# Performance work log

Hardware: AMD Instinct MI355X
Metric: run time of the kernel (lower is better)

Reference implementation:

```python
import jax, jax.numpy as jnp
import numpy as np

# SLAYER SRM-alpha kernel: k[n] = (n/tau) * exp(1 - n/tau), k[0] = 0 (Ts = 1).
# Realized exactly as a 2-state linear recurrence instead of an explicit time conv:
#   s1[n] = r*s1[n-1] + x[n];  s2[n] = r*s2[n-1] + r*s1[n];  out[n] = (e/tau)*s2[n-1]
# which reproduces k[n] = n * r**n * e / tau for an impulse.

def _alpha_psp(x, tau):
    r = jnp.float32(np.exp(-1.0 / tau))
    coef = jnp.float32(np.e / tau)
    xT = jnp.moveaxis(x, -1, 0)  # [T,N,C,H,W]
    zeros = jnp.zeros_like(xT[0])
    def step(carry, xt):
        s1, s2 = carry
        out = coef * s2          # kernel value 0 at lag 0
        s1 = r * s1 + xt
        s2 = r * s2 + r * s1
        return (s1, s2), out
    _, out = jax.lax.scan(step, (zeros, zeros), xT)
    return jnp.moveaxis(out, 0, -1)


def _make_spike_fn(theta, tauRho, scaleRho):
    # Hard threshold forward, SLAYER exponential surrogate backward.
    @jax.custom_vjp
    def f(u):
        return (u >= theta).astype(u.dtype)
    def fwd(u):
        return f(u), u
    def bwd(u, g):
        pdf = (scaleRho / tauRho) * jnp.exp(-jnp.abs(u - theta) / (tauRho * theta))
        return (g * pdf,)
    f.defvjp(fwd, bwd)
    return f


def _spike_dynamics(u, theta, tauRef, scaleRef, tauRho, scaleRho):
    # membrane[t] = u[t] + refractory response of past spikes,
    # refKernel[n] = -scaleRef*theta * (n/tauRef) * exp(1 - n/tauRef)
    r = jnp.float32(np.exp(-1.0 / tauRef))
    coef = jnp.float32(-scaleRef * theta * np.e / tauRef)
    spike_fn = _make_spike_fn(theta, tauRho, scaleRho)
    uT = jnp.moveaxis(u, -1, 0)  # [T,N,C,H,W]
    zeros = jnp.zeros_like(uT[0])
    def step(carry, ut):
        s1, s2 = carry
        m = ut + coef * s2       # spike at t does not refract itself (kernel[0]=0)
        s = spike_fn(m)
        s1 = r * s1 + s
        s2 = r * s2 + r * s1
        return (s1, s2), s
    _, out = jax.lax.scan(step, (zeros, zeros), uT)
    return jnp.moveaxis(out, 0, -1)


def _conv2d_time(x, w, pad):
    # SLAYER conv3d with kernel (k,k,1): a 2D conv applied independently per timestep.
    N, C, H, W, T = x.shape
    xb = jnp.moveaxis(x, -1, 1).reshape(N * T, C, H, W)
    y = jax.lax.conv_general_dilated(
        xb, w, (1, 1), [(pad, pad), (pad, pad)],
        dimension_numbers=('NCHW', 'OIHW', 'NCHW'))
    return jnp.moveaxis(y.reshape(N, T, w.shape[0], H, W), 1, -1)


def setup_inputs() -> dict:
    key = jax.random.key(0)
    k1, k2, k3, k4 = jax.random.split(key, 4)
    N, C, H, W, T = 8, 4, 128, 128, 50
    spikeInput = (jax.random.uniform(k1, (N, C, H, W, T)) < 0.1).astype(jnp.float32)
    # weight scales chosen so membranes cross the per-layer thresholds (SLAYER weightScale)
    w1 = jax.random.normal(k2, (4, 4, 5, 5), jnp.float32) * 2.0
    w2 = jax.random.normal(k3, (4, 4, 3, 3), jnp.float32) * 4.0
    w3 = jax.random.normal(k4, (4, 4, 3, 3), jnp.float32) * 8.0
    return {"spikeInput": spikeInput, "w1": w1, "w2": w2, "w3": w3}


def reference(spikeInput, w1, w2, w3):
    s1 = _spike_dynamics(_conv2d_time(_alpha_psp(spikeInput, 1.0), w1, 2),
                         20.0, 1.0, 1.0, 1.0, 10.0)
    s2 = _spike_dynamics(_conv2d_time(_alpha_psp(s1, 2.0), w2, 1),
                         40.0, 2.0, 1.0, 1.0, 10.0)
    # Layer 3 is computed by the original forward but its result is NOT returned
    # (the torch code returns spikes_layer_2). XLA will DCE it.
    s3 = _spike_dynamics(_conv2d_time(_alpha_psp(s2, 4.0), w3, 1),
                         80.0, 4.0, 1.0, 10.0, 100.0)
    return s2
```

## Files before the change

kernel.cpp:

```cpp
#include <hip/hip_runtime.h>


#define TC 10

__global__ __launch_bounds__(256)
void snn_pack(const float* __restrict__ xin, uint2* __restrict__ xmg)
{
    __shared__ unsigned long long bal[4][50];
    const int tid  = threadIdx.x;
    const int lane = tid & 63;
    const int ws   = tid >> 6;
    const size_t wpx = ((size_t)blockIdx.x * 4 + ws) * 64;
    const float* src = xin + wpx * 50;
#pragma unroll 1
    for (int j = 0; j < 50; ++j) {
        float v = src[j * 64 + lane];
        unsigned long long b = __ballot(v != 0.f);
        if (lane == 0) bal[ws][j] = b;
    }
    __syncthreads();
    const int bitpos = lane * 50;
    const int w = bitpos >> 6, s = bitpos & 63;
    unsigned long long m = bal[ws][w] >> s;
    if (s > 14) m |= bal[ws][w + 1] << (64 - s);
    m &= (1ull << 50) - 1;
    xmg[wpx + lane] = make_uint2((unsigned)m, (unsigned)(m >> 32));
}

#define HS1 20
#define HP1 21
__global__ __launch_bounds__(256)
void snn_l1(const uint2* __restrict__ xmg, const float* __restrict__ w1,
            uint2* __restrict__ s1g)
{
    __shared__ __align__(16) uint2 xs[4][HS1 * HP1];
    __shared__ __align__(16) float wL1[400];

    const int tid = threadIdx.x;
    const int n = blockIdx.z, Y0 = blockIdx.y * 16, X0 = blockIdx.x * 16;

    for (int i = tid; i < 400; i += 256) {
        int oc = i & 3, r = i >> 2;
        int ic = r / 25, r2 = r - ic * 25;
        int dy = r2 / 5, dx = r2 - dy * 5;
        wL1[i] = w1[((oc * 4 + ic) * 5 + dy) * 5 + dx];
    }
#pragma unroll
    for (int s = 0; s < 2; ++s) {
        int hp = tid + s * 256;
        if (hp < HS1 * HS1) {
            int hy = hp / HS1, hx = hp - hy * HS1;
            int gy = Y0 + hy - 2, gx = X0 + hx - 2;
            bool ok = gy >= 0 && gy < 128 && gx >= 0 && gx < 128;
            int gi = (gy << 7) + gx;
            int li = hy * HP1 + hx;
#pragma unroll
            for (int c = 0; c < 4; ++c) {
                uint2 v = make_uint2(0u, 0u);
                if (ok) v = xmg[(((size_t)(n * 4 + c)) << 14) + gi];
                xs[c][li] = v;
            }
        }
    }
    __syncthreads();

    const int cy = tid >> 4, cx = tid & 15;
    const int base = cy * HP1 + cx;

    float s1a[4] = {}, s2a[4] = {}, s1b[4] = {}, s2b[4] = {};
    unsigned long long om[4] = {};
    const float R1  = 0.36787944117144233f;
    const float CO1 = 2.7182818284590452f;
    const float CRF = -54.365636569180902f;

    for (int chk = 0; chk < 5; ++chk) {
        const int t0 = chk * TC;
        float a[TC][4];
#pragma unroll
        for (int u = 0; u < TC; ++u) { a[u][0]=0.f; a[u][1]=0.f; a[u][2]=0.f; a[u][3]=0.f; }
#pragma unroll 1
        for (int ic = 0; ic < 4; ++ic) {
            const uint2*  xp = &xs[ic][base];
            const float4* wp = (const float4*)&wL1[ic * 100];
#pragma unroll 1
            for (int dy = 0; dy < 5; ++dy) {
#pragma unroll
                for (int dx = 0; dx < 5; ++dx) {
                    uint2 mv = xp[dx];
                    unsigned long long mm = ((unsigned long long)mv.y << 32) | mv.x;
                    unsigned win = (unsigned)(mm >> t0);
                    float4 w = wp[dx];
#pragma unroll
                    for (int u = 0; u < TC; ++u) {
                        float f = (float)((win >> u) & 1u);
                        a[u][0] = fmaf(f, w.x, a[u][0]);
                        a[u][1] = fmaf(f, w.y, a[u][1]);
                        a[u][2] = fmaf(f, w.z, a[u][2]);
                        a[u][3] = fmaf(f, w.w, a[u][3]);
                    }
                }
                xp += HP1; wp += 5;
            }
        }
        unsigned cm[4] = {0, 0, 0, 0};
#pragma unroll
        for (int u = 0; u < TC; ++u) {
#pragma unroll
            for (int oc = 0; oc < 4; ++oc) {
                float ao  = CO1 * s2a[oc];
                float ns1 = fmaf(R1, s1a[oc], a[u][oc]);
                s1a[oc] = ns1;
                s2a[oc] = fmaf(R1, s2a[oc], R1 * ns1);
                float mv = fmaf(CRF, s2b[oc], ao);
                unsigned b = (mv >= 20.f) ? 1u : 0u;
                float spf = (float)b;
                float nb1 = fmaf(R1, s1b[oc], spf);
                s1b[oc] = nb1;
                s2b[oc] = fmaf(R1, s2b[oc], R1 * nb1);
                cm[oc] |= b << u;
            }
        }
#pragma unroll
        for (int oc = 0; oc < 4; ++oc)
            om[oc] |= (unsigned long long)cm[oc] << t0;
    }

    const int yx = (Y0 + cy) * 128 + X0 + cx;
#pragma unroll
    for (int oc = 0; oc < 4; ++oc)
        s1g[(((size_t)(n * 4 + oc)) << 14) + yx] =
            make_uint2((unsigned)om[oc], (unsigned)(om[oc] >> 32));
}

#define HS2 18
#define HP2 19
__global__ __launch_bounds__(256)
void snn_l2(const uint2* __restrict__ s1g, const float* __restrict__ w2,
            float* __restrict__ out)
{
    __shared__ __align__(16) uint2 ss[4][HS2 * HP2];
    __shared__ __align__(16) float wL2[144];
    __shared__ unsigned long long oml[256 * 4];

    const int tid = threadIdx.x;
    const int n = blockIdx.z, Y0 = blockIdx.y * 16, X0 = blockIdx.x * 16;

    if (tid < 144) {
        int oc = tid & 3, r = tid >> 2;
        int ic = r / 9, r2 = r - ic * 9;
        int dy = r2 / 3, dx = r2 - dy * 3;
        wL2[tid] = w2[((oc * 4 + ic) * 3 + dy) * 3 + dx];
    }
#pragma unroll
    for (int s = 0; s < 2; ++s) {
        int hp = tid + s * 256;
        if (hp < HS2 * HS2) {
            int hy = hp / HS2, hx = hp - hy * HS2;
            int gy = Y0 + hy - 1, gx = X0 + hx - 1;
            bool ok = gy >= 0 && gy < 128 && gx >= 0 && gx < 128;
            int gi = (gy << 7) + gx;
            int li = hy * HP2 + hx;
#pragma unroll
            for (int c = 0; c < 4; ++c) {
                uint2 v = make_uint2(0u, 0u);
                if (ok) v = s1g[(((size_t)(n * 4 + c)) << 14) + gi];
                ss[c][li] = v;
            }
        }
    }
    __syncthreads();

    const int cy = tid >> 4, cx = tid & 15;
    const int base = cy * HP2 + cx;

    float s1c[4] = {}, s2c[4] = {}, s1d[4] = {}, s2d[4] = {};
    unsigned long long om[4] = {};
    const float R2  = 0.60653065971263342f;
    const float CO2 = 1.3591409142295226f;
    const float CRF = -54.365636569180902f;

    for (int chk = 0; chk < 5; ++chk) {
        const int t0 = chk * TC;
        float a[TC][4];
#pragma unroll
        for (int u = 0; u < TC; ++u) { a[u][0]=0.f; a[u][1]=0.f; a[u][2]=0.f; a[u][3]=0.f; }
#pragma unroll 1
        for (int ic = 0; ic < 4; ++ic) {
            const uint2*  sp = &ss[ic][base];
            const float4* wp = (const float4*)&wL2[ic * 36];
#pragma unroll 1
            for (int dy = 0; dy < 3; ++dy) {
#pragma unroll
                for (int dx = 0; dx < 3; ++dx) {
                    uint2 mv = sp[dx];
                    unsigned long long mm = ((unsigned long long)mv.y << 32) | mv.x;
                    unsigned win = (unsigned)(mm >> t0);
                    float4 w = wp[dx];
#pragma unroll
                    for (int u = 0; u < TC; ++u) {
                        float f = (float)((win >> u) & 1u);
                        a[u][0] = fmaf(f, w.x, a[u][0]);
                        a[u][1] = fmaf(f, w.y, a[u][1]);
                        a[u][2] = fmaf(f, w.z, a[u][2]);
                        a[u][3] = fmaf(f, w.w, a[u][3]);
                    }
                }
                sp += HP2; wp += 3;
            }
        }
        unsigned cm[4] = {0, 0, 0, 0};
#pragma unroll
        for (int u = 0; u < TC; ++u) {
#pragma unroll
            for (int oc = 0; oc < 4; ++oc) {
                float ao  = CO2 * s2c[oc];
                float ns1 = fmaf(R2, s1c[oc], a[u][oc]);
                s1c[oc] = ns1;
                s2c[oc] = fmaf(R2, s2c[oc], R2 * ns1);
                float mv = fmaf(CRF, s2d[oc], ao);
                unsigned b = (mv >= 40.f) ? 1u : 0u;
                float spf = (float)b;
                float nd1 = fmaf(R2, s1d[oc], spf);
                s1d[oc] = nd1;
                s2d[oc] = fmaf(R2, s2d[oc], R2 * nd1);
                cm[oc] |= b << u;
            }
        }
#pragma unroll
        for (int oc = 0; oc < 4; ++oc)
            om[oc] |= (unsigned long long)cm[oc] << t0;
    }

#pragma unroll
    for (int oc = 0; oc < 4; ++oc) oml[tid * 4 + oc] = om[oc];
    __syncthreads();

    for (int i = tid; i < 256 * 4 * 25; i += 256) {
        int pc = i / 25;
        int j  = i - pc * 25;
        int p  = pc >> 2, c = pc & 3;
        unsigned long long m = oml[p * 4 + c];
        int py = p >> 4, px = p & 15;
        int k = 2 * j;
        float2 v;
        v.x = (float)((unsigned)(m >> k) & 1u);
        v.y = (float)((unsigned)(m >> (k + 1)) & 1u);
        float* o = out + ((size_t)(((n * 4 + c) << 14) + (Y0 + py) * 128 + X0 + px)) * 50;
        *(float2*)(o + k) = v;
    }
}

#define TW   16
#define TH   8
#define R1S  (TW + 6)
#define R1R  (TH + 6)
#define R1N  (R1S * R1R)
#define R2S  (TW + 2)
#define R2R  (TH + 2)
#define R2N  (R2S * R2R)

__global__ __launch_bounds__(256)
void snn_fused_fb(const float* __restrict__ xin,
                  const float* __restrict__ w1,
                  const float* __restrict__ w2,
                  float* __restrict__ out)
{
    __shared__ __align__(16) uint2    xm[4][R1N];
    __shared__ unsigned               s1m[4][R2N];
    __shared__ __align__(16) float    wL1[400];
    __shared__ __align__(16) float    wL2[144];

    const int tid = threadIdx.x;
    const int n   = blockIdx.z;
    const int Y0  = blockIdx.y * TH;
    const int X0  = blockIdx.x * TW;

    for (int i = tid; i < 400; i += 256) {
        int oc = i & 3, r = i >> 2;
        int ic = r / 25, r2 = r - ic * 25;
        int dy = r2 / 5, dx = r2 - dy * 5;
        wL1[i] = w1[((oc * 4 + ic) * 5 + dy) * 5 + dx];
    }
    if (tid < 144) {
        int oc = tid & 3, r = tid >> 2;
        int ic = r / 9, r2 = r - ic * 9;
        int dy = r2 / 3, dx = r2 - dy * 3;
        wL2[tid] = w2[((oc * 4 + ic) * 3 + dy) * 3 + dx];
    }
#pragma unroll
    for (int s = 0; s < 2; ++s) {
        int hp = tid + s * 256;
        if (hp < R1N) {
            int hy = hp / R1S, hx = hp - hy * R1S;
            int gy = Y0 + hy - 3, gx = X0 + hx - 3;
            bool inimg = gy >= 0 && gy < 128 && gx >= 0 && gx < 128;
#pragma unroll
            for (int c = 0; c < 4; ++c) {
                unsigned m0 = 0, m1 = 0;
                if (inimg) {
                    const float2* p = (const float2*)
                        (xin + ((size_t)(((n * 4 + c) * 128 + gy) * 128 + gx)) * 50);
#pragma unroll
                    for (int j = 0; j < 25; ++j) {
                        float2 v = p[j];
                        unsigned b0 = (v.x != 0.f) ? 1u : 0u;
                        unsigned b1 = (v.y != 0.f) ? 1u : 0u;
                        int k = 2 * j;
                        if (k < 32) m0 |= (b0 << k) | (b1 << (k + 1));
                        else        m1 |= (b0 << (k - 32)) | (b1 << (k - 31));
                    }
                }
                xm[c][hp] = make_uint2(m0, m1);
            }
        }
    }
    const bool cw = (tid < R2N);
    const int cy = tid / R2S;
    const int cx = tid - cy * R2S;
    const bool cin = cw && (Y0 + cy - 1) >= 0 && (Y0 + cy - 1) < 128
                        && (X0 + cx - 1) >= 0 && (X0 + cx - 1) < 128;
    const int xbase = cy * R1S + cx;
    const bool iw = (tid < TW * TH);
    const int iy = tid >> 4, ix = tid & 15;
    const int ibase = iy * R2S + ix;

    float s1a[4] = {}, s2a[4] = {}, s1b[4] = {}, s2b[4] = {};
    float s1c[4] = {}, s2c[4] = {}, s1d[4] = {}, s2d[4] = {};
    unsigned long long om[4] = {};

    const float R1  = 0.36787944117144233f;
    const float CO1 = 2.7182818284590452f;
    const float R2  = 0.60653065971263342f;
    const float CO2 = 1.3591409142295226f;
    const float CRF = -54.365636569180902f;

    __syncthreads();

    for (int chk = 0; chk < 5; ++chk) {
        const int t0 = chk * TC;
        if (cw) {
            float a[TC][4];
#pragma unroll
            for (int u = 0; u < TC; ++u) { a[u][0]=0.f; a[u][1]=0.f; a[u][2]=0.f; a[u][3]=0.f; }
            if (cin) {
#pragma unroll 1
                for (int ic = 0; ic < 4; ++ic) {
                    const uint2*  xp = &xm[ic][xbase];
                    const float4* wp = (const float4*)&wL1[ic * 100];
#pragma unroll 1
                    for (int dy = 0; dy < 5; ++dy) {
#pragma unroll
                        for (int dx = 0; dx < 5; ++dx) {
                            uint2 m = xp[dx];
                            unsigned long long mm =
                                ((unsigned long long)m.y << 32) | m.x;
                            unsigned win = (unsigned)(mm >> t0);
                            float4 w = wp[dx];
#pragma unroll
                            for (int u = 0; u < TC; ++u) {
                                float f = (float)((win >> u) & 1u);
                                a[u][0] = fmaf(f, w.x, a[u][0]);
                                a[u][1] = fmaf(f, w.y, a[u][1]);
                                a[u][2] = fmaf(f, w.z, a[u][2]);
                                a[u][3] = fmaf(f, w.w, a[u][3]);
                            }
                        }
                        xp += R1S; wp += 5;
                    }
                }
            }
            unsigned cm[4] = {0, 0, 0, 0};
#pragma unroll
            for (int u = 0; u < TC; ++u) {
#pragma unroll
                for (int oc = 0; oc < 4; ++oc) {
                    float ao  = CO1 * s2a[oc];
                    float ns1 = fmaf(R1, s1a[oc], a[u][oc]);
                    s1a[oc] = ns1;
                    s2a[oc] = fmaf(R1, s2a[oc], R1 * ns1);
                    float mv = fmaf(CRF, s2b[oc], ao);
                    unsigned b = (mv >= 20.f) ? 1u : 0u;
                    float spf = (float)b;
                    float nb1 = fmaf(R1, s1b[oc], spf);
                    s1b[oc] = nb1;
                    s2b[oc] = fmaf(R1, s2b[oc], R1 * nb1);
                    cm[oc] |= b << u;
                }
            }
            s1m[0][tid] = cm[0];
            s1m[1][tid] = cm[1];
            s1m[2][tid] = cm[2];
            s1m[3][tid] = cm[3];
        }
        __syncthreads();
        if (iw) {
            float a[TC][4];
#pragma unroll
            for (int u = 0; u < TC; ++u) { a[u][0]=0.f; a[u][1]=0.f; a[u][2]=0.f; a[u][3]=0.f; }
#pragma unroll 1
            for (int ic = 0; ic < 4; ++ic) {
                const unsigned* sp = &s1m[ic][ibase];
                const float4*   wp = (const float4*)&wL2[ic * 36];
#pragma unroll 1
                for (int dy = 0; dy < 3; ++dy) {
#pragma unroll
                    for (int dx = 0; dx < 3; ++dx) {
                        unsigned win = sp[dx];
                        float4 w = wp[dx];
#pragma unroll
                        for (int u = 0; u < TC; ++u) {
                            float f = (float)((win >> u) & 1u);
                            a[u][0] = fmaf(f, w.x, a[u][0]);
                            a[u][1] = fmaf(f, w.y, a[u][1]);
                            a[u][2] = fmaf(f, w.z, a[u][2]);
                            a[u][3] = fmaf(f, w.w, a[u][3]);
                        }
                    }
                    sp += R2S; wp += 3;
                }
            }
            unsigned cm[4] = {0, 0, 0, 0};
#pragma unroll
            for (int u = 0; u < TC; ++u) {
#pragma unroll
                for (int oc = 0; oc < 4; ++oc) {
                    float ao  = CO2 * s2c[oc];
                    float ns1 = fmaf(R2, s1c[oc], a[u][oc]);
                    s1c[oc] = ns1;
                    s2c[oc] = fmaf(R2, s2c[oc], R2 * ns1);
                    float mv = fmaf(CRF, s2d[oc], ao);
                    unsigned b = (mv >= 40.f) ? 1u : 0u;
                    float spf = (float)b;
                    float nd1 = fmaf(R2, s1d[oc], spf);
                    s1d[oc] = nd1;
                    s2d[oc] = fmaf(R2, s2d[oc], R2 * nd1);
                    cm[oc] |= b << u;
                }
            }
#pragma unroll
            for (int oc = 0; oc < 4; ++oc)
                om[oc] |= (unsigned long long)cm[oc] << t0;
        }
        __syncthreads();
    }
    if (iw) {
#pragma unroll
        for (int c = 0; c < 4; ++c) {
            float* p = out + ((size_t)(((n * 4 + c) * 128 + (Y0 + iy)) * 128 + (X0 + ix))) * 50;
            unsigned long long m = om[c];
#pragma unroll
            for (int j = 0; j < 25; ++j) {
                int k = 2 * j;
                float2 v;
                v.x = (float)((unsigned)(m >> k) & 1u);
                v.y = (float)((unsigned)(m >> (k + 1)) & 1u);
                *(float2*)(p + k) = v;
            }
        }
    }
}

extern "C" void kernel_launch(void* const* d_in, const int* in_sizes, int n_in,
                              void* d_out, int out_size, void* d_ws, size_t ws_size,
                              hipStream_t stream) {
    (void)in_sizes; (void)n_in; (void)out_size;
    const float* x  = (const float*)d_in[0];
    const float* w1 = (const float*)d_in[1];
    const float* w2 = (const float*)d_in[2];
    float* o = (float*)d_out;

    if (ws_size >= 2u * 4194304u) {
        uint2* xmg = (uint2*)d_ws;
        uint2* s1g = xmg + 524288;
        hipLaunchKernelGGL(snn_pack, dim3(2048), dim3(256), 0, stream, x, xmg);
        hipLaunchKernelGGL(snn_l1, dim3(8, 8, 8), dim3(256), 0, stream, xmg, w1, s1g);
        hipLaunchKernelGGL(snn_l2, dim3(8, 8, 8), dim3(256), 0, stream, s1g, w2, o);
    } else {
        dim3 grid(128 / TW, 128 / TH, 8);
        hipLaunchKernelGGL(snn_fused_fb, grid, dim3(256), 0, stream, x, w1, w2, o);
    }
}
```

Measured before the change: 326.3 us.

## Split input channels across thread pairs and double grid in conv layers

Each pixel in the layer-1 and layer-2 kernels is now handled by two threads. Each thread convolves two of the four input channels, and the partial sums are exchanged with a lane shuffle. Each thread then runs the recurrence for two output channels. Tiles shrink to 16x8 and the grid doubles, so there are more blocks and more waves to hide latency on the 512-block launch. The cost is extra shuffles and more halo reloading per output pixel.

```diff
diff --git a/kernel.cpp b/kernel.cpp
--- a/kernel.cpp
+++ b/kernel.cpp
@@ -27,17 +27,18 @@
     xmg[wpx + lane] = make_uint2((unsigned)m, (unsigned)(m >> 32));
 }
 
-#define HS1 20
+#define HW1 20
+#define HH1 12
 #define HP1 21
 __global__ __launch_bounds__(256)
 void snn_l1(const uint2* __restrict__ xmg, const float* __restrict__ w1,
             uint2* __restrict__ s1g)
 {
-    __shared__ __align__(16) uint2 xs[4][HS1 * HP1];
+    __shared__ __align__(16) uint2 xs[4][HH1 * HP1];
     __shared__ __align__(16) float wL1[400];
 
     const int tid = threadIdx.x;
-    const int n = blockIdx.z, Y0 = blockIdx.y * 16, X0 = blockIdx.x * 16;
+    const int n = blockIdx.z, Y0 = blockIdx.y * 8, X0 = blockIdx.x * 16;
 
     for (int i = tid; i < 400; i += 256) {
         int oc = i & 3, r = i >> 2;
@@ -45,11 +46,10 @@
         int dy = r2 / 5, dx = r2 - dy * 5;
         wL1[i] = w1[((oc * 4 + ic) * 5 + dy) * 5 + dx];
     }
-#pragma unroll
-    for (int s = 0; s < 2; ++s) {
-        int hp = tid + s * 256;
-        if (hp < HS1 * HS1) {
-            int hy = hp / HS1, hx = hp - hy * HS1;
+    {
+        int hp = tid;
+        if (hp < HW1 * HH1) {
+            int hy = hp / HW1, hx = hp - hy * HW1;
             int gy = Y0 + hy - 2, gx = X0 + hx - 2;
             bool ok = gy >= 0 && gy < 128 && gx >= 0 && gx < 128;
             int gi = (gy << 7) + gx;
@@ -64,11 +64,13 @@
     }
     __syncthreads();
 
-    const int cy = tid >> 4, cx = tid & 15;
-    const int base = cy * HP1 + cx;
-
-    float s1a[4] = {}, s2a[4] = {}, s1b[4] = {}, s2b[4] = {};
-    unsigned long long om[4] = {};
+    const int h  = tid & 1;
+    const int px = tid >> 1;
+    const int py = px >> 4, pxx = px & 15;
+    const int base = py * HP1 + pxx;
+
+    float s1a[2] = {}, s2a[2] = {}, s1b[2] = {}, s2b[2] = {};
+    unsigned long long om[2] = {};
     const float R1  = 0.36787944117144233f;
     const float CO1 = 2.7182818284590452f;
     const float CRF = -54.365636569180902f;
@@ -79,7 +81,8 @@
 #pragma unroll
         for (int u = 0; u < TC; ++u) { a[u][0]=0.f; a[u][1]=0.f; a[u][2]=0.f; a[u][3]=0.f; }
 #pragma unroll 1
-        for (int ic = 0; ic < 4; ++ic) {
+        for (int icl = 0; icl < 2; ++icl) {
+            const int ic = 2 * h + icl;
             const uint2*  xp = &xs[ic][base];
             const float4* wp = (const float4*)&wL1[ic * 100];
 #pragma unroll 1
@@ -102,48 +105,67 @@
                 xp += HP1; wp += 5;
             }
         }
-        unsigned cm[4] = {0, 0, 0, 0};
+        unsigned cm0 = 0, cm1 = 0;
 #pragma unroll
         for (int u = 0; u < TC; ++u) {
-#pragma unroll
-            for (int oc = 0; oc < 4; ++oc) {
-                float ao  = CO1 * s2a[oc];
-                float ns1 = fmaf(R1, s1a[oc], a[u][oc]);
-                s1a[oc] = ns1;
-                s2a[oc] = fmaf(R1, s2a[oc], R1 * ns1);
-                float mv = fmaf(CRF, s2b[oc], ao);
-                unsigned b = (mv >= 20.f) ? 1u : 0u;
-                float spf = (float)b;
-                float nb1 = fmaf(R1, s1b[oc], spf);
-                s1b[oc] = nb1;
-                s2b[oc] = fmaf(R1, s2b[oc], R1 * nb1);
-                cm[oc] |= b << u;
-            }
-        }
-#pragma unroll
-        for (int oc = 0; oc < 4; ++oc)
-            om[oc] |= (unsigned long long)cm[oc] << t0;
-    }
-
-    const int yx = (Y0 + cy) * 128 + X0 + cx;
-#pragma unroll
-    for (int oc = 0; oc < 4; ++oc)
+            float give0 = h ? a[u][0] : a[u][2];
+            float give1 = h ? a[u][1] : a[u][3];
+            float got0 = __shfl_xor(give0, 1);
+            float got1 = __shfl_xor(give1, 1);
+            float mine0 = h ? a[u][2] : a[u][0];
+            float mine1 = h ? a[u][3] : a[u][1];
+            float c0 = mine0 + got0;
+            float c1 = mine1 + got1;
+            float ao0  = CO1 * s2a[0];
+            float ns10 = fmaf(R1, s1a[0], c0);
+            s1a[0] = ns10;
+            s2a[0] = fmaf(R1, s2a[0], R1 * ns10);
+            float mv0 = fmaf(CRF, s2b[0], ao0);
+            unsigned b0 = (mv0 >= 20.f) ? 1u : 0u;
+            float sp0 = (float)b0;
+            float nb10 = fmaf(R1, s1b[0], sp0);
+            s1b[0] = nb10;
+            s2b[0] = fmaf(R1, s2b[0], R1 * nb10);
+            cm0 |= b0 << u;
+
+            float ao1  = CO1 * s2a[1];
+            float ns11 = fmaf(R1, s1a[1], c1);
+            s1a[1] = ns11;
+            s2a[1] = fmaf(R1, s2a[1], R1 * ns11);
+            float mv1 = fmaf(CRF, s2b[1], ao1);
+            unsigned b1 = (mv1 >= 20.f) ? 1u : 0u;
+            float sp1 = (float)b1;
+            float nb11 = fmaf(R1, s1b[1], sp1);
+            s1b[1] = nb11;
+            s2b[1] = fmaf(R1, s2b[1], R1 * nb11);
+            cm1 |= b1 << u;
+        }
+        om[0] |= (unsigned long long)cm0 << t0;
+        om[1] |= (unsigned long long)cm1 << t0;
+    }
+
+    const int yx = (Y0 + py) * 128 + X0 + pxx;
+#pragma unroll
+    for (int j = 0; j < 2; ++j) {
+        int oc = 2 * h + j;
         s1g[(((size_t)(n * 4 + oc)) << 14) + yx] =
-            make_uint2((unsigned)om[oc], (unsigned)(om[oc] >> 32));
+            make_uint2((unsigned)om[j], (unsigned)(om[j] >> 32));
+    }
 }
 
-#define HS2 18
+#define HW2 18
+#define HH2 10
 #define HP2 19
 __global__ __launch_bounds__(256)
 void snn_l2(const uint2* __restrict__ s1g, const float* __restrict__ w2,
             float* __restrict__ out)
 {
-    __shared__ __align__(16) uint2 ss[4][HS2 * HP2];
+    __shared__ __align__(16) uint2 ss[4][HH2 * HP2];
     __shared__ __align__(16) float wL2[144];
-    __shared__ unsigned long long oml[256 * 4];
+    __shared__ unsigned long long oml[128 * 4];
 
     const int tid = threadIdx.x;
-    const int n = blockIdx.z, Y0 = blockIdx.y * 16, X0 = blockIdx.x * 16;
+    const int n = blockIdx.z, Y0 = blockIdx.y * 8, X0 = blockIdx.x * 16;
 
     if (tid < 144) {
         int oc = tid & 3, r = tid >> 2;
@@ -151,11 +173,10 @@
         int dy = r2 / 3, dx = r2 - dy * 3;
         wL2[tid] = w2[((oc * 4 + ic) * 3 + dy) * 3 + dx];
     }
-#pragma unroll
-    for (int s = 0; s < 2; ++s) {
-        int hp = tid + s * 256;
-        if (hp < HS2 * HS2) {
-            int hy = hp / HS2, hx = hp - hy * HS2;
+    {
+        int hp = tid;
+        if (hp < HW2 * HH2) {
+            int hy = hp / HW2, hx = hp - hy * HW2;
             int gy = Y0 + hy - 1, gx = X0 + hx - 1;
             bool ok = gy >= 0 && gy < 128 && gx >= 0 && gx < 128;
             int gi = (gy << 7) + gx;
@@ -170,11 +191,13 @@
     }
     __syncthreads();
 
-    const int cy = tid >> 4, cx = tid & 15;
-    const int base = cy * HP2 + cx;
-
-    float s1c[4] = {}, s2c[4] = {}, s1d[4] = {}, s2d[4] = {};
-    unsigned long long om[4] = {};
+    const int h  = tid & 1;
+    const int px = tid >> 1;
+    const int py = px >> 4, pxx = px & 15;
+    const int base = py * HP2 + pxx;
+
+    float s1c[2] = {}, s2c[2] = {}, s1d[2] = {}, s2d[2] = {};
+    unsigned long long om[2] = {};
     const float R2  = 0.60653065971263342f;
     const float CO2 = 1.3591409142295226f;
     const float CRF = -54.365636569180902f;
@@ -185,7 +208,8 @@
 #pragma unroll
         for (int u = 0; u < TC; ++u) { a[u][0]=0.f; a[u][1]=0.f; a[u][2]=0.f; a[u][3]=0.f; }
 #pragma unroll 1
-        for (int ic = 0; ic < 4; ++ic) {
+        for (int icl = 0; icl < 2; ++icl) {
+            const int ic = 2 * h + icl;
             const uint2*  sp = &ss[ic][base];
             const float4* wp = (const float4*)&wL2[ic * 36];
 #pragma unroll 1
@@ -208,44 +232,61 @@
                 sp += HP2; wp += 3;
             }
         }
-        unsigned cm[4] = {0, 0, 0, 0};
+        unsigned cm0 = 0, cm1 = 0;
 #pragma unroll
         for (int u = 0; u < TC; ++u) {
-#pragma unroll
-            for (int oc = 0; oc < 4; ++oc) {
-                float ao  = CO2 * s2c[oc];
-                float ns1 = fmaf(R2, s1c[oc], a[u][oc]);
-                s1c[oc] = ns1;
-                s2c[oc] = fmaf(R2, s2c[oc], R2 * ns1);
-                float mv = fmaf(CRF, s2d[oc], ao);
-                unsigned b = (mv >= 40.f) ? 1u : 0u;
-                float spf = (float)b;
-                float nd1 = fmaf(R2, s1d[oc], spf);
-                s1d[oc] = nd1;
-                s2d[oc] = fmaf(R2, s2d[oc], R2 * nd1);
-                cm[oc] |= b << u;
-            }
-        }
-#pragma unroll
-        for (int oc = 0; oc < 4; ++oc)
-            om[oc] |= (unsigned long long)cm[oc] << t0;
-    }
-
-#pragma unroll
-    for (int oc = 0; oc < 4; ++oc) oml[tid * 4 + oc] = om[oc];
+            float give0 = h ? a[u][0] : a[u][2];
+            float give1 = h ? a[u][1] : a[u][3];
+            float got0 = __shfl_xor(give0, 1);
+            float got1 = __shfl_xor(give1, 1);
+            float mine0 = h ? a[u][2] : a[u][0];
+            float mine1 = h ? a[u][3] : a[u][1];
+            float c0 = mine0 + got0;
+            float c1 = mine1 + got1;
+
+            float ao0  = CO2 * s2c[0];
+            float ns10 = fmaf(R2, s1c[0], c0);
+            s1c[0] = ns10;
+            s2c[0] = fmaf(R2, s2c[0], R2 * ns10);
+            float mv0 = fmaf(CRF, s2d[0], ao0);
+            unsigned b0 = (mv0 >= 40.f) ? 1u : 0u;
+            float sp0 = (float)b0;
+            float nd10 = fmaf(R2, s1d[0], sp0);
+            s1d[0] = nd10;
+            s2d[0] = fmaf(R2, s2d[0], R2 * nd10);
+            cm0 |= b0 << u;
+
+            float ao1  = CO2 * s2c[1];
+            float ns11 = fmaf(R2, s1c[1], c1);
+            s1c[1] = ns11;
+            s2c[1] = fmaf(R2, s2c[1], R2 * ns11);
+            float mv1 = fmaf(CRF, s2d[1], ao1);
+            unsigned b1 = (mv1 >= 40.f) ? 1u : 0u;
+            float sp1 = (float)b1;
+            float nd11 = fmaf(R2, s1d[1], sp1);
+            s1d[1] = nd11;
+            s2d[1] = fmaf(R2, s2d[1], R2 * nd11);
+            cm1 |= b1 << u;
+        }
+        om[0] |= (unsigned long long)cm0 << t0;
+        om[1] |= (unsigned long long)cm1 << t0;
+    }
+
+    oml[px * 4 + 2 * h]     = om[0];
+    oml[px * 4 + 2 * h + 1] = om[1];
     __syncthreads();
 
-    for (int i = tid; i < 256 * 4 * 25; i += 256) {
+    for (int i = tid; i < 128 * 4 * 25; i += 256) {
         int pc = i / 25;
         int j  = i - pc * 25;
         int p  = pc >> 2, c = pc & 3;
-        unsigned long long m = oml[p * 4 + c];
-        int py = p >> 4, px = p & 15;
+        unsigned long long m = oml[pc];
+        int py2 = p >> 4, px2 = p & 15;
         int k = 2 * j;
         float2 v;
         v.x = (float)((unsigned)(m >> k) & 1u);
         v.y = (float)((unsigned)(m >> (k + 1)) & 1u);
-        float* o = out + ((size_t)(((n * 4 + c) << 14) + (Y0 + py) * 128 + X0 + px)) * 50;
+        float* o = out + ((size_t)(((n * 4 + c) << 14) + (Y0 + py2) * 128 + X0 + px2)) * 50;
         *(float2*)(o + k) = v;
     }
 }
@@ -473,8 +514,8 @@
         uint2* xmg = (uint2*)d_ws;
         uint2* s1g = xmg + 524288;
         hipLaunchKernelGGL(snn_pack, dim3(2048), dim3(256), 0, stream, x, xmg);
-        hipLaunchKernelGGL(snn_l1, dim3(8, 8, 8), dim3(256), 0, stream, xmg, w1, s1g);
-        hipLaunchKernelGGL(snn_l2, dim3(8, 8, 8), dim3(256), 0, stream, s1g, w2, o);
+        hipLaunchKernelGGL(snn_l1, dim3(8, 16, 8), dim3(256), 0, stream, xmg, w1, s1g);
+        hipLaunchKernelGGL(snn_l2, dim3(8, 16, 8), dim3(256), 0, stream, s1g, w2, o);
     } else {
         dim3 grid(128 / TW, 128 / TH, 8);
         hipLaunchKernelGGL(snn_fused_fb, grid, dim3(256), 0, stream, x, w1, w2, o);
```

New measurement: 324.8 us. No clear change (-0.5%).
